# Kernel optimization log

Measured on AMD Instinct MI355X. Metric: run time of the kernel, lower is better.

The kernel has to match this reference:

```python
import jax, jax.numpy as jnp
import numpy as np

QUANT_LIMIT = 127.0  # 2**(8-1) - 1, signed int8


def _quantize(x, amax):
    # per-tensor symmetric int8 quantization: round(clip(x * 127/amax, -127, 127))
    s = QUANT_LIMIT / amax
    return jnp.round(jnp.clip(x * s, -QUANT_LIMIT, QUANT_LIMIT))


def setup_inputs() -> dict:
    key = jax.random.key(0)
    kx, kw, kb = jax.random.split(key, 3)
    B, S, K, N = 4, 2048, 4096, 4096
    x = jax.random.normal(kx, (B, S, K), dtype=jnp.float32)
    weight = jax.random.normal(kw, (N, K), dtype=jnp.float32) * 0.03  # kaiming-ish scale
    bias = jax.random.normal(kb, (N,), dtype=jnp.float32) * 0.01
    amax = jnp.float32(4.0)     # calibrated activation amax for N(0,1)
    amax_w = jnp.float32(0.12)  # calibrated weight amax
    return {"x": x, "weight": weight, "bias": bias, "amax": amax, "amax_w": amax_w}


def reference(x, weight, bias, amax, amax_w):
    # quantize to int8
    qx = _quantize(x, amax).astype(jnp.int8)           # [B,S,K]
    qw = _quantize(weight, amax_w).astype(jnp.int8)    # [N,K]
    # int8 matmul with int32 accumulation (exact-accumulation variant of the
    # approximate-multiplier kernel)
    acc = jnp.einsum("bsk,nk->bsn", qx.astype(jnp.int32), qw.astype(jnp.int32))
    # rescale: output = acc / ((127/amax) * (127/amax_w)), then bias add
    scale = (QUANT_LIMIT / amax) * (QUANT_LIMIT / amax_w)
    out = acc.astype(jnp.float32) / scale + bias
    return out
```

## Files before the change

kernel.cpp:

```cpp
#include <hip/hip_runtime.h>
#include <stdint.h>

typedef __attribute__((ext_vector_type(4))) int i32x4;

#define QLIM 127.0f

__global__ __launch_bounds__(256) void quantize_fused(
    const float4* __restrict__ x, const float4* __restrict__ w,
    int* __restrict__ q,
    const float* __restrict__ amax, const float* __restrict__ amax_w,
    long nx4, long ntot4)
{
    const float sx = QLIM / amax[0];
    const float sw = QLIM / amax_w[0];
    const long stride = (long)gridDim.x * blockDim.x;
    for (long i = (long)blockIdx.x * blockDim.x + threadIdx.x; i < ntot4; i += stride) {
        const bool isx = i < nx4;
        const float4 v = isx ? x[i] : w[i - nx4];
        const float s  = isx ? sx : sw;
        float a0 = rintf(fminf(fmaxf(v.x * s, -QLIM), QLIM));
        float a1 = rintf(fminf(fmaxf(v.y * s, -QLIM), QLIM));
        float a2 = rintf(fminf(fmaxf(v.z * s, -QLIM), QLIM));
        float a3 = rintf(fminf(fmaxf(v.w * s, -QLIM), QLIM));
        q[i] = ((int)a0 & 255) | (((int)a1 & 255) << 8) |
               (((int)a2 & 255) << 16) | (((int)a3 & 255) << 24);
    }
}


#define STAGE(mat, tt, kh) do {                                              \
    if ((tt) < nt) {                                                         \
        const size_t go = (size_t)((tt) * 128 + (kh) * 64);                  \
        const int ld = ((((tt) & 1) << 15) | ((kh) << 14));                  \
        __builtin_amdgcn_global_load_lds(                                    \
            (const __attribute__((address_space(1))) void*)(mat##Src + go),  \
            (__attribute__((address_space(3))) void*)(lds + mat##Dst + ld),  \
            16, 0, 0);                                                       \
        __builtin_amdgcn_global_load_lds(                                    \
            (const __attribute__((address_space(1))) void*)(mat##Src + go + rowStep), \
            (__attribute__((address_space(3))) void*)(lds + mat##Dst + ld + 8192),    \
            16, 0, 0);                                                       \
    }                                                                        \
} while (0)

__global__ __launch_bounds__(512, 2) void gemm_i8_8phase(
    const signed char* __restrict__ A,
    const signed char* __restrict__ B,
    const float* __restrict__ bias,
    const float* __restrict__ amax,
    const float* __restrict__ amax_w,
    float* __restrict__ C,
    int M, int N, int K)
{
    __shared__ signed char lds[131072];

    const int tid  = threadIdx.x;
    const int wid  = tid >> 6;
    const int lane = tid & 63;
    const int wr   = wid >> 2;
    const int wc   = wid & 3;
    const int bn   = blockIdx.x;
    const int bm   = blockIdx.y;
    const int nt   = K >> 7;

    const int fr   = lane & 15;
    const int fk   = (lane >> 4) << 4;
    const int fswz = ((fr >> 1) & 3) << 4;

    const int aRd = (wr * 128 + fr) * 64 + (fk ^ fswz);
    const int bRd = 65536 + (wc * 64 + fr) * 64 + (fk ^ fswz);

    const int srow = tid >> 2;
    const int csw  = (((tid & 3) ^ ((tid >> 3) & 3)) << 4);
    const signed char* aSrc = A + (size_t)(bm * 256 + srow) * K + csw;
    const signed char* bSrc = B + (size_t)(bn * 256 + srow) * K + csw;
    const size_t rowStep = (size_t)128 * K;
    const int aDst = wid << 10;
    const int bDst = 65536 + (wid << 10);

    i32x4 acc[8][4] = {};

    STAGE(a, 0, 0); STAGE(b, 0, 0); STAGE(a, 0, 1); STAGE(b, 0, 1);
    STAGE(a, 1, 0); STAGE(b, 1, 0);
    asm volatile("s_waitcnt vmcnt(4)" ::: "memory");
    __builtin_amdgcn_s_barrier();

#pragma unroll 1
    for (int t = 0; t < nt; ++t) {
        const int bb = (t & 1) << 15;
        const signed char* pa = lds + bb + aRd;
        const signed char* pb = lds + bb + bRd;
        i32x4 af[4], bf[4];

#pragma unroll
        for (int mm = 0; mm < 4; ++mm) af[mm] = *(const i32x4*)(pa + mm * 1024);
#pragma unroll
        for (int nn = 0; nn < 4; ++nn) bf[nn] = *(const i32x4*)(pb + nn * 1024);
        STAGE(a, t + 1, 1);
        __builtin_amdgcn_s_barrier();
        asm volatile("s_waitcnt lgkmcnt(0)" ::: "memory");
        __builtin_amdgcn_sched_barrier(0);
        __builtin_amdgcn_s_setprio(1);
#pragma unroll
        for (int mm = 0; mm < 4; ++mm)
#pragma unroll
            for (int nn = 0; nn < 4; ++nn)
                acc[mm][nn] = __builtin_amdgcn_mfma_i32_16x16x64_i8(af[mm], bf[nn], acc[mm][nn], 0, 0, 0);
        __builtin_amdgcn_s_setprio(0);
        __builtin_amdgcn_s_barrier();

#pragma unroll
        for (int mm = 0; mm < 4; ++mm) af[mm] = *(const i32x4*)(pa + 4096 + mm * 1024);
        STAGE(b, t + 1, 1);
        __builtin_amdgcn_s_barrier();
        asm volatile("s_waitcnt lgkmcnt(0)" ::: "memory");
        __builtin_amdgcn_sched_barrier(0);
        __builtin_amdgcn_s_setprio(1);
#pragma unroll
        for (int mm = 0; mm < 4; ++mm)
#pragma unroll
            for (int nn = 0; nn < 4; ++nn)
                acc[4 + mm][nn] = __builtin_amdgcn_mfma_i32_16x16x64_i8(af[mm], bf[nn], acc[4 + mm][nn], 0, 0, 0);
        __builtin_amdgcn_s_setprio(0);
        __builtin_amdgcn_s_barrier();

#pragma unroll
        for (int mm = 0; mm < 4; ++mm) af[mm] = *(const i32x4*)(pa + 16384 + mm * 1024);
#pragma unroll
        for (int nn = 0; nn < 4; ++nn) bf[nn] = *(const i32x4*)(pb + 16384 + nn * 1024);
        STAGE(a, t + 2, 0);
        __builtin_amdgcn_s_barrier();
        asm volatile("s_waitcnt lgkmcnt(0)" ::: "memory");
        __builtin_amdgcn_sched_barrier(0);
        __builtin_amdgcn_s_setprio(1);
#pragma unroll
        for (int mm = 0; mm < 4; ++mm)
#pragma unroll
            for (int nn = 0; nn < 4; ++nn)
                acc[mm][nn] = __builtin_amdgcn_mfma_i32_16x16x64_i8(af[mm], bf[nn], acc[mm][nn], 0, 0, 0);
        __builtin_amdgcn_s_setprio(0);
        __builtin_amdgcn_s_barrier();

#pragma unroll
        for (int mm = 0; mm < 4; ++mm) af[mm] = *(const i32x4*)(pa + 16384 + 4096 + mm * 1024);
        STAGE(b, t + 2, 0);
        __builtin_amdgcn_s_barrier();
        asm volatile("s_waitcnt lgkmcnt(0)" ::: "memory");
        __builtin_amdgcn_sched_barrier(0);
        __builtin_amdgcn_s_setprio(1);
#pragma unroll
        for (int mm = 0; mm < 4; ++mm)
#pragma unroll
            for (int nn = 0; nn < 4; ++nn)
                acc[4 + mm][nn] = __builtin_amdgcn_mfma_i32_16x16x64_i8(af[mm], bf[nn], acc[4 + mm][nn], 0, 0, 0);
        __builtin_amdgcn_s_setprio(0);
        if (t < nt - 2) asm volatile("s_waitcnt vmcnt(4)" ::: "memory");
        else            asm volatile("s_waitcnt vmcnt(0)" ::: "memory");
        __builtin_amdgcn_s_barrier();
    }

    const float sa  = QLIM / amax[0];
    const float sw  = QLIM / amax_w[0];
    const float inv = 1.0f / (sa * sw);
    const int row0 = bm * 256 + wr * 128;
    const int col0 = bn * 256 + wc * 64;
    const int rsub = (lane >> 4) << 2;
#pragma unroll
    for (int m = 0; m < 8; ++m) {
#pragma unroll
        for (int n = 0; n < 4; ++n) {
            const int colc = col0 + n * 16 + fr;
            const float bv = bias[colc];
#pragma unroll
            for (int r = 0; r < 4; ++r) {
                const int rowc = row0 + m * 16 + rsub + r;
                C[(size_t)rowc * N + colc] = (float)acc[m][n][r] * inv + bv;
            }
        }
    }
}

extern "C" void kernel_launch(void* const* d_in, const int* in_sizes, int n_in,
                              void* d_out, int out_size, void* d_ws, size_t ws_size,
                              hipStream_t stream) {
    const float* x      = (const float*)d_in[0];
    const float* w      = (const float*)d_in[1];
    const float* bias   = (const float*)d_in[2];
    const float* amax   = (const float*)d_in[3];
    const float* amax_w = (const float*)d_in[4];
    float* out = (float*)d_out;

    const int N = in_sizes[2];
    const int K = in_sizes[1] / N;
    const int M = in_sizes[0] / K;

    signed char* qx = (signed char*)d_ws;
    signed char* qw = qx + (size_t)M * K;

    const long nx4   = (long)M * K / 4;
    const long ntot4 = nx4 + (long)N * K / 4;
    quantize_fused<<<2048, 256, 0, stream>>>((const float4*)x, (const float4*)w,
                                             (int*)qx, amax, amax_w, nx4, ntot4);

    dim3 grid(N / 256, M / 256);
    gemm_i8_8phase<<<grid, 512, 0, stream>>>(qx, qw, bias, amax, amax_w, out, M, N, K);
}
```

Before: 405.9 us.

## Collapse four-phase k-loop into two phases and stage epilogue through LDS

Each k-tile half now loads all eight A fragments and four B fragments at once and issues 32 MFMAs per phase. This halves the barriers and waitcnt points per iteration but raises register pressure. The epilogue writes the scaled and biased results into swizzled LDS in two halves, then writes float4 rows out to global memory. The goal is coalesced stores in place of scattered 4-byte writes.

```diff
diff --git a/kernel.cpp b/kernel.cpp
--- a/kernel.cpp
+++ b/kernel.cpp
@@ -43,7 +43,7 @@
     }                                                                        \
 } while (0)
 
-__global__ __launch_bounds__(512, 2) void gemm_i8_8phase(
+__global__ __launch_bounds__(512, 2) void gemm_i8_2phase(
     const signed char* __restrict__ A,
     const signed char* __restrict__ B,
     const float* __restrict__ bias,
@@ -90,19 +90,20 @@
         const int bb = (t & 1) << 15;
         const signed char* pa = lds + bb + aRd;
         const signed char* pb = lds + bb + bRd;
-        i32x4 af[4], bf[4];
+        i32x4 af[8], bf[4];
 
 #pragma unroll
-        for (int mm = 0; mm < 4; ++mm) af[mm] = *(const i32x4*)(pa + mm * 1024);
+        for (int mm = 0; mm < 8; ++mm) af[mm] = *(const i32x4*)(pa + mm * 1024);
 #pragma unroll
         for (int nn = 0; nn < 4; ++nn) bf[nn] = *(const i32x4*)(pb + nn * 1024);
         STAGE(a, t + 1, 1);
+        STAGE(b, t + 1, 1);
         __builtin_amdgcn_s_barrier();
         asm volatile("s_waitcnt lgkmcnt(0)" ::: "memory");
         __builtin_amdgcn_sched_barrier(0);
         __builtin_amdgcn_s_setprio(1);
 #pragma unroll
-        for (int mm = 0; mm < 4; ++mm)
+        for (int mm = 0; mm < 8; ++mm)
 #pragma unroll
             for (int nn = 0; nn < 4; ++nn)
                 acc[mm][nn] = __builtin_amdgcn_mfma_i32_16x16x64_i8(af[mm], bf[nn], acc[mm][nn], 0, 0, 0);
@@ -110,49 +111,20 @@
         __builtin_amdgcn_s_barrier();
 
 #pragma unroll
-        for (int mm = 0; mm < 4; ++mm) af[mm] = *(const i32x4*)(pa + 4096 + mm * 1024);
-        STAGE(b, t + 1, 1);
-        __builtin_amdgcn_s_barrier();
-        asm volatile("s_waitcnt lgkmcnt(0)" ::: "memory");
-        __builtin_amdgcn_sched_barrier(0);
-        __builtin_amdgcn_s_setprio(1);
-#pragma unroll
-        for (int mm = 0; mm < 4; ++mm)
-#pragma unroll
-            for (int nn = 0; nn < 4; ++nn)
-                acc[4 + mm][nn] = __builtin_amdgcn_mfma_i32_16x16x64_i8(af[mm], bf[nn], acc[4 + mm][nn], 0, 0, 0);
-        __builtin_amdgcn_s_setprio(0);
-        __builtin_amdgcn_s_barrier();
-
-#pragma unroll
-        for (int mm = 0; mm < 4; ++mm) af[mm] = *(const i32x4*)(pa + 16384 + mm * 1024);
+        for (int mm = 0; mm < 8; ++mm) af[mm] = *(const i32x4*)(pa + 16384 + mm * 1024);
 #pragma unroll
         for (int nn = 0; nn < 4; ++nn) bf[nn] = *(const i32x4*)(pb + 16384 + nn * 1024);
         STAGE(a, t + 2, 0);
-        __builtin_amdgcn_s_barrier();
-        asm volatile("s_waitcnt lgkmcnt(0)" ::: "memory");
-        __builtin_amdgcn_sched_barrier(0);
-        __builtin_amdgcn_s_setprio(1);
-#pragma unroll
-        for (int mm = 0; mm < 4; ++mm)
-#pragma unroll
-            for (int nn = 0; nn < 4; ++nn)
-                acc[mm][nn] = __builtin_amdgcn_mfma_i32_16x16x64_i8(af[mm], bf[nn], acc[mm][nn], 0, 0, 0);
-        __builtin_amdgcn_s_setprio(0);
-        __builtin_amdgcn_s_barrier();
-
-#pragma unroll
-        for (int mm = 0; mm < 4; ++mm) af[mm] = *(const i32x4*)(pa + 16384 + 4096 + mm * 1024);
         STAGE(b, t + 2, 0);
         __builtin_amdgcn_s_barrier();
         asm volatile("s_waitcnt lgkmcnt(0)" ::: "memory");
         __builtin_amdgcn_sched_barrier(0);
         __builtin_amdgcn_s_setprio(1);
 #pragma unroll
-        for (int mm = 0; mm < 4; ++mm)
+        for (int mm = 0; mm < 8; ++mm)
 #pragma unroll
             for (int nn = 0; nn < 4; ++nn)
-                acc[4 + mm][nn] = __builtin_amdgcn_mfma_i32_16x16x64_i8(af[mm], bf[nn], acc[4 + mm][nn], 0, 0, 0);
+                acc[mm][nn] = __builtin_amdgcn_mfma_i32_16x16x64_i8(af[mm], bf[nn], acc[mm][nn], 0, 0, 0);
         __builtin_amdgcn_s_setprio(0);
         if (t < nt - 2) asm volatile("s_waitcnt vmcnt(4)" ::: "memory");
         else            asm volatile("s_waitcnt vmcnt(0)" ::: "memory");
@@ -162,20 +134,36 @@
     const float sa  = QLIM / amax[0];
     const float sw  = QLIM / amax_w[0];
     const float inv = 1.0f / (sa * sw);
-    const int row0 = bm * 256 + wr * 128;
-    const int col0 = bn * 256 + wc * 64;
+    float* ldsf = (float*)lds;
     const int rsub = (lane >> 4) << 2;
+
+#pragma unroll 1
+    for (int h = 0; h < 2; ++h) {
+        __builtin_amdgcn_s_barrier();
 #pragma unroll
-    for (int m = 0; m < 8; ++m) {
+        for (int mq = 0; mq < 4; ++mq) {
 #pragma unroll
-        for (int n = 0; n < 4; ++n) {
-            const int colc = col0 + n * 16 + fr;
-            const float bv = bias[colc];
+            for (int n = 0; n < 4; ++n) {
+                const int colc = wc * 64 + n * 16 + fr;
+                const float bv = bias[bn * 256 + colc];
 #pragma unroll
-            for (int r = 0; r < 4; ++r) {
-                const int rowc = row0 + m * 16 + rsub + r;
-                C[(size_t)rowc * N + colc] = (float)acc[m][n][r] * inv + bv;
+                for (int r = 0; r < 4; ++r) {
+                    const int lrow = wr * 64 + mq * 16 + rsub + r;
+                    const int pc = colc ^ ((lrow & 12) << 2);
+                    ldsf[lrow * 256 + pc] = (float)acc[h * 4 + mq][n][r] * inv + bv;
+                }
             }
+        }
+        __builtin_amdgcn_s_barrier();
+#pragma unroll
+        for (int it = 0; it < 16; ++it) {
+            const int i = it * 512 + tid;
+            const int lrow = i >> 6;
+            const int lc = i & 63;
+            const int pc4 = lc ^ (lrow & 12);
+            const float4 v = *(const float4*)(ldsf + lrow * 256 + pc4 * 4);
+            const int grow = bm * 256 + (lrow >> 6) * 128 + h * 64 + (lrow & 63);
+            *(float4*)(C + (size_t)grow * N + bn * 256 + lc * 4) = v;
         }
     }
 }
@@ -203,5 +191,5 @@
                                              (int*)qx, amax, amax_w, nx4, ntot4);
 
     dim3 grid(N / 256, M / 256);
-    gemm_i8_8phase<<<grid, 512, 0, stream>>>(qx, qw, bias, amax, amax_w, out, M, N, K);
+    gemm_i8_2phase<<<grid, 512, 0, stream>>>(qx, qw, bias, amax, amax_w, out, M, N, K);
 }
```

Result: slower. 475.4 us (+17.1%).
